# Optimization experiments

Hardware: AMD Instinct MI355X
Metric: run time of the kernel (lower is better)

## Reference

```python
import jax, jax.numpy as jnp
import numpy as np

B, S, D, H = 4, 8192, 256, 8

def setup_inputs() -> dict:
    key = jax.random.key(0)
    ks = jax.random.split(key, 6)
    return {
        "q": jax.random.normal(ks[0], (B, S, D), dtype=jnp.float32),
        "k": jax.random.normal(ks[1], (B, S, D), dtype=jnp.float32),
        "v": jax.random.normal(ks[2], (B, S, D), dtype=jnp.float32),
        "q_weights": jax.random.normal(ks[3], (H, D, D), dtype=jnp.float32),
        "k_weights": jax.random.normal(ks[4], (H, D, D), dtype=jnp.float32),
        "v_weights": jax.random.normal(ks[5], (H, D, D), dtype=jnp.float32),
    }

def reference(q, k, v, q_weights, k_weights, v_weights):
    # Faithful to the original: einsum 'bsd,hio->bhsd' shares no index between
    # the activation and the weight, so it is q[b,s,d] * sum_{i,o} W[h,i,o].
    qs = jax.nn.softmax(jnp.einsum('bsd,hio->bhsd', q, q_weights), axis=-2)  # softmax over s
    ks = jax.nn.softmax(jnp.einsum('bsd,hio->bhsd', k, k_weights), axis=-2)
    vs = jnp.einsum('bsd,hio->bhsd', v, v_weights)
    # 'bhnk,bhmv->bhkv': n and m are independently summed (outer product of seq-sums)
    global_contexts = jnp.einsum('bhnk,bhmv->bhkv', ks, vs)  # [b,h,d,d]
    # 'bhkv,bhsq->bhsv': k and q independently summed
    out = jnp.einsum('bhkv,bhsq->bhsv', global_contexts, qs)  # [b,h,s,d]
    # AdaptiveMaxPool2d((D,1)) on layout 'b s d h': identity over d (d==D), max over heads
    out = jnp.max(out, axis=1)  # [b,s,d]
    return out
```

## Files before the change

kernel.cpp:

```cpp
#include <hip/hip_runtime.h>

#define B 4
#define S 8192
#define D 256
#define H 8
#define NT 128
#define LOG2E 1.4426950408889634f
#define E2(x) __builtin_amdgcn_exp2f(x)

#define WS_WQ    0
#define WS_WV    8
#define WS_QMAX  16
#define WS_QMIN  (WS_QMAX + B*D)
#define WS_CV    (WS_QMIN + B*D)
#define WS_ZACC  (WS_CV + B*D)
#define WS_WP    (WS_ZACC + B*H*D)
#define WS_P1    (WS_WP + 1024)
#define WS_P2    (WS_P1 + B*NT*D)
#define WS_P3    (WS_P2 + B*NT*D)

__global__ __launch_bounds__(256) void kA(const float* __restrict__ q,
                                          const float* __restrict__ v,
                                          const float* __restrict__ qw,
                                          const float* __restrict__ vw,
                                          float* __restrict__ ws) {
    const int blk = blockIdx.x;
    const int t = threadIdx.x, w = t >> 6, lane = t & 63;

    if (blk >= B * NT) {
        const int i = blk - B * NT;
        const float4* src = (const float4*)(((i >> 7) ? vw : qw)
                              + (size_t)((i >> 4) & 7) * D * D) + (i & 15) * 1024;
        float sm = 0.f;
        #pragma unroll
        for (int j = 0; j < 4; ++j) {
            float4 a4 = src[j * 256 + t];
            sm += (a4.x + a4.y) + (a4.z + a4.w);
        }
        #pragma unroll
        for (int off = 32; off; off >>= 1) sm += __shfl_down(sm, off, 64);
        if (lane == 0) ws[WS_WP + i * 4 + w] = sm;
        return;
    }

    const int b = blk >> 7, tl = blk & (NT - 1);
    const int g = lane >> 4, cl = lane & 15;
    const int cblk = w * 16 + cl;
    const float4* qbase = (const float4*)(q + ((size_t)b * S + tl * 64) * D);
    const float4* vbase = (const float4*)(v + ((size_t)b * S + tl * 64) * D);
    float4 qmx = make_float4(-3.4e38f, -3.4e38f, -3.4e38f, -3.4e38f);
    float4 qmn = make_float4(3.4e38f, 3.4e38f, 3.4e38f, 3.4e38f);
    float4 vs = make_float4(0.f, 0.f, 0.f, 0.f);
    #pragma unroll 4
    for (int i = 0; i < 16; ++i) {
        const int row = i * 4 + g;
        float4 a4 = qbase[row * 64 + cblk];
        qmx.x = fmaxf(qmx.x, a4.x); qmx.y = fmaxf(qmx.y, a4.y);
        qmx.z = fmaxf(qmx.z, a4.z); qmx.w = fmaxf(qmx.w, a4.w);
        qmn.x = fminf(qmn.x, a4.x); qmn.y = fminf(qmn.y, a4.y);
        qmn.z = fminf(qmn.z, a4.z); qmn.w = fminf(qmn.w, a4.w);
        float4 b4 = vbase[row * 64 + cblk];
        vs.x += b4.x; vs.y += b4.y; vs.z += b4.z; vs.w += b4.w;
    }
    #pragma unroll
    for (int off = 16; off <= 32; off <<= 1) {
        qmx.x = fmaxf(qmx.x, __shfl_xor(qmx.x, off, 64));
        qmx.y = fmaxf(qmx.y, __shfl_xor(qmx.y, off, 64));
        qmx.z = fmaxf(qmx.z, __shfl_xor(qmx.z, off, 64));
        qmx.w = fmaxf(qmx.w, __shfl_xor(qmx.w, off, 64));
        qmn.x = fminf(qmn.x, __shfl_xor(qmn.x, off, 64));
        qmn.y = fminf(qmn.y, __shfl_xor(qmn.y, off, 64));
        qmn.z = fminf(qmn.z, __shfl_xor(qmn.z, off, 64));
        qmn.w = fminf(qmn.w, __shfl_xor(qmn.w, off, 64));
        vs.x += __shfl_xor(vs.x, off, 64);
        vs.y += __shfl_xor(vs.y, off, 64);
        vs.z += __shfl_xor(vs.z, off, 64);
        vs.w += __shfl_xor(vs.w, off, 64);
    }
    if (g == 0) {
        size_t pi = (size_t)(b * NT + tl) * D + cblk * 4;
        *(float4*)&ws[WS_P1 + pi] = qmx;
        *(float4*)&ws[WS_P2 + pi] = qmn;
        *(float4*)&ws[WS_P3 + pi] = vs;
    }
}

__global__ __launch_bounds__(256) void kB(float* __restrict__ ws) {
    const int blk = blockIdx.x, t = threadIdx.x;
    if (blk < 32) {
        const int bb = blk >> 3, oct = blk & 7;
        const int dl = t >> 3, sub = t & 7;
        const int d = oct * 32 + dl;
        float mx = -3.4e38f, mn = 3.4e38f, sm = 0.f;
        #pragma unroll 4
        for (int i = 0; i < 16; ++i) {
            size_t idx = (size_t)(bb * NT + sub * 16 + i) * D + d;
            mx = fmaxf(mx, ws[WS_P1 + idx]);
            mn = fminf(mn, ws[WS_P2 + idx]);
            sm += ws[WS_P3 + idx];
        }
        #pragma unroll
        for (int off = 1; off < 8; off <<= 1) {
            mx = fmaxf(mx, __shfl_xor(mx, off, 64));
            mn = fminf(mn, __shfl_xor(mn, off, 64));
            sm += __shfl_xor(sm, off, 64);
        }
        if (sub == 0) {
            ws[WS_QMAX + bb * D + d] = mx;
            ws[WS_QMIN + bb * D + d] = mn;
            ws[WS_CV + bb * D + d] = sm * (float)D;
        }
    } else if (blk == 32) {
        const int o = t >> 4, j = t & 15;
        float s = 0.f;
        #pragma unroll
        for (int ww = 0; ww < 4; ++ww) s += ws[WS_WP + (o * 16 + j) * 4 + ww];
        #pragma unroll
        for (int off = 1; off < 16; off <<= 1) s += __shfl_xor(s, off, 16);
        if (j == 0) ws[(o >= 8) ? (WS_WV + o - 8) : (WS_WQ + o)] = s;
    } else {
        #pragma unroll
        for (int e = 0; e < 8; ++e)
            *(float4*)&ws[WS_ZACC + e * 1024 + t * 4] = make_float4(0.f, 0.f, 0.f, 0.f);
    }
}

__global__ __launch_bounds__(256) void kC(const float* __restrict__ q,
                                          float* __restrict__ ws) {
    const int blk = blockIdx.x;
    const int b = blk >> 7, c = blk & 127;
    const int d = threadIdx.x;
    const float qmx = ws[WS_QMAX + b * D + d];
    const float qmn = ws[WS_QMIN + b * D + d];
    float a[H], cc[H], z[H];
    #pragma unroll
    for (int h = 0; h < H; ++h) {
        float wq_ = ws[WS_WQ + h];
        float M = (wq_ >= 0.f) ? wq_ * qmx : wq_ * qmn;
        a[h] = wq_ * LOG2E;
        cc[h] = -M * LOG2E;
        z[h] = 0.f;
    }
    const float* qp = q + ((size_t)b * S + c * 64) * D + d;
    #pragma unroll 4
    for (int r = 0; r < 64; ++r) {
        float qv = qp[(size_t)r * D];
        #pragma unroll
        for (int h = 0; h < H; ++h) z[h] += E2(fmaf(qv, a[h], cc[h]));
    }
    #pragma unroll
    for (int h = 0; h < H; ++h)
        atomicAdd(&ws[WS_ZACC + (size_t)(b * H + h) * D + d], z[h]);
}

__global__ __launch_bounds__(256, 8) void kE(const float* __restrict__ q,
                                             const float* __restrict__ ws,
                                             float* __restrict__ out) {
    __shared__ float kcs[H * D];
    __shared__ float wvs[8];

    const int blk = blockIdx.x;
    const int b = blk >> 9, tl = blk & 511;
    const int t = threadIdx.x, w = t >> 6, lane = t & 63;
    const int r = t >> 4, slice = t & 15;

    const float4* qp = (const float4*)(q + ((size_t)b * S + tl * 16 + r) * D
                                       + slice * 16);
    const float4 q0 = qp[0], q1 = qp[1], q2 = qp[2], q3 = qp[3];

    const int dst = ((t >> 2) & 3) * 64 + (t >> 4) * 4 + (t & 3);
    const float qmx = ws[WS_QMAX + b * D + t];
    const float qmn = ws[WS_QMIN + b * D + t];
    float a[H];
    #pragma unroll
    for (int h = 0; h < H; ++h) {
        const float wq_ = ws[WS_WQ + h];
        const float M = (wq_ >= 0.f) ? wq_ * qmx : wq_ * qmn;
        kcs[h * 256 + dst] = -M * LOG2E
            - __builtin_amdgcn_logf(ws[WS_ZACC + (size_t)(b * H + h) * D + t]);
        a[h] = wq_ * LOG2E;
    }
    if (t < 8) wvs[t] = ws[WS_WV + t];
    const float4 cv4 = *(const float4*)&ws[WS_CV + b * D + lane * 4];
    __syncthreads();

    float p[H];
    #pragma unroll
    for (int h = 0; h < H; ++h) p[h] = 0.f;

    const float4* kc4 = (const float4*)kcs;
    #pragma unroll
    for (int j = 0; j < 4; ++j) {
        const float4 qv = (j == 0) ? q0 : (j == 1) ? q1 : (j == 2) ? q2 : q3;
        #pragma unroll
        for (int h = 0; h < H; ++h) {
            const float4 k = kc4[h * 64 + j * 16 + slice];
            p[h] += (E2(fmaf(qv.x, a[h], k.x)) + E2(fmaf(qv.y, a[h], k.y)))
                  + (E2(fmaf(qv.z, a[h], k.z)) + E2(fmaf(qv.w, a[h], k.w)));
        }
    }
    #pragma unroll
    for (int st = 1; st < 16; st <<= 1) {
        #pragma unroll
        for (int h = 0; h < H; ++h) p[h] += __shfl_xor(p[h], st, 16);
    }
    float amax = -3.4e38f, amin = 3.4e38f;
    #pragma unroll
    for (int h = 0; h < H; ++h) {
        const float A = wvs[h] * p[h];
        amax = fmaxf(amax, A);
        amin = fminf(amin, A);
    }

    float* og = out + ((size_t)b * S + tl * 16 + w * 4) * D;
    #pragma unroll
    for (int rr = 0; rr < 4; ++rr) {
        const float am = __shfl(amax, rr * 16, 64);
        const float an = __shfl(amin, rr * 16, 64);
        float4 o;
        o.x = (cv4.x >= 0.f) ? cv4.x * am : cv4.x * an;
        o.y = (cv4.y >= 0.f) ? cv4.y * am : cv4.y * an;
        o.z = (cv4.z >= 0.f) ? cv4.z * am : cv4.z * an;
        o.w = (cv4.w >= 0.f) ? cv4.w * am : cv4.w * an;
        *(float4*)&og[(size_t)rr * D + lane * 4] = o;
    }
}

extern "C" void kernel_launch(void* const* d_in, const int* in_sizes, int n_in,
                              void* d_out, int out_size, void* d_ws, size_t ws_size,
                              hipStream_t stream) {
    const float* q  = (const float*)d_in[0];
    const float* v  = (const float*)d_in[2];
    const float* qw = (const float*)d_in[3];
    const float* vw = (const float*)d_in[5];
    float* out = (float*)d_out;
    float* ws  = (float*)d_ws;

    kA<<<B * NT + 256, 256, 0, stream>>>(q, v, qw, vw, ws);
    kB<<<34, 256, 0, stream>>>(ws);
    kC<<<512, 256, 0, stream>>>(q, ws);
    kE<<<B * 512, 256, 0, stream>>>(q, ws, out);
}
```

Before: 51.69 us.

## Replace reduction kernel with order-preserving atomics and double rows per block in kE

Drops the separate reduction kernel kB: kA now folds per-tile q max/min into global results with atomicMax on an order-preserving unsigned encoding of floats, and folds v sums and weight sums with atomicAdd. A memset zeroes the accumulators first. kE now handles 32 rows per block in two groups, reusing the per-block shared setup (log of the normalizers) across twice as many rows. The trade is atomic contention on a small set of addresses and more work per block in kE, with fewer blocks in flight.

```diff
diff --git a/kernel.cpp b/kernel.cpp
--- a/kernel.cpp
+++ b/kernel.cpp
@@ -4,20 +4,24 @@
 #define S 8192
 #define D 256
 #define H 8
-#define NT 128
 #define LOG2E 1.4426950408889634f
 #define E2(x) __builtin_amdgcn_exp2f(x)
 
 #define WS_WQ    0
 #define WS_WV    8
-#define WS_QMAX  16
-#define WS_QMIN  (WS_QMAX + B*D)
-#define WS_CV    (WS_QMIN + B*D)
+#define WS_QMAXE 16
+#define WS_QMINE (WS_QMAXE + B*D)
+#define WS_CV    (WS_QMINE + B*D)
 #define WS_ZACC  (WS_CV + B*D)
-#define WS_WP    (WS_ZACC + B*H*D)
-#define WS_P1    (WS_WP + 1024)
-#define WS_P2    (WS_P1 + B*NT*D)
-#define WS_P3    (WS_P2 + B*NT*D)
+#define WS_END   (WS_ZACC + B*H*D)
+
+__device__ __forceinline__ unsigned enc(float x) {
+    unsigned u = __float_as_uint(x);
+    return (u >> 31) ? ~u : (u | 0x80000000u);
+}
+__device__ __forceinline__ float dec(unsigned e) {
+    return (e >> 31) ? __uint_as_float(e & 0x7FFFFFFFu) : __uint_as_float(~e);
+}
 
 __global__ __launch_bounds__(256) void kA(const float* __restrict__ q,
                                           const float* __restrict__ v,
@@ -27,10 +31,11 @@
     const int blk = blockIdx.x;
     const int t = threadIdx.x, w = t >> 6, lane = t & 63;
 
-    if (blk >= B * NT) {
-        const int i = blk - B * NT;
+    if (blk >= 512) {
+        const int i = blk - 512;
+        const int h = (i >> 4) & 7;
         const float4* src = (const float4*)(((i >> 7) ? vw : qw)
-                              + (size_t)((i >> 4) & 7) * D * D) + (i & 15) * 1024;
+                              + (size_t)h * D * D) + (i & 15) * 1024;
         float sm = 0.f;
         #pragma unroll
         for (int j = 0; j < 4; ++j) {
@@ -39,11 +44,16 @@
         }
         #pragma unroll
         for (int off = 32; off; off >>= 1) sm += __shfl_down(sm, off, 64);
-        if (lane == 0) ws[WS_WP + i * 4 + w] = sm;
+        __shared__ float red[4];
+        if (lane == 0) red[w] = sm;
+        __syncthreads();
+        if (t == 0)
+            atomicAdd(&ws[((i >> 7) ? WS_WV : WS_WQ) + h],
+                      (red[0] + red[1]) + (red[2] + red[3]));
         return;
     }
 
-    const int b = blk >> 7, tl = blk & (NT - 1);
+    const int b = blk >> 7, tl = blk & 127;
     const int g = lane >> 4, cl = lane & 15;
     const int cblk = w * 16 + cl;
     const float4* qbase = (const float4*)(q + ((size_t)b * S + tl * 64) * D);
@@ -78,50 +88,17 @@
         vs.w += __shfl_xor(vs.w, off, 64);
     }
     if (g == 0) {
-        size_t pi = (size_t)(b * NT + tl) * D + cblk * 4;
-        *(float4*)&ws[WS_P1 + pi] = qmx;
-        *(float4*)&ws[WS_P2 + pi] = qmn;
-        *(float4*)&ws[WS_P3 + pi] = vs;
-    }
-}
-
-__global__ __launch_bounds__(256) void kB(float* __restrict__ ws) {
-    const int blk = blockIdx.x, t = threadIdx.x;
-    if (blk < 32) {
-        const int bb = blk >> 3, oct = blk & 7;
-        const int dl = t >> 3, sub = t & 7;
-        const int d = oct * 32 + dl;
-        float mx = -3.4e38f, mn = 3.4e38f, sm = 0.f;
-        #pragma unroll 4
-        for (int i = 0; i < 16; ++i) {
-            size_t idx = (size_t)(bb * NT + sub * 16 + i) * D + d;
-            mx = fmaxf(mx, ws[WS_P1 + idx]);
-            mn = fminf(mn, ws[WS_P2 + idx]);
-            sm += ws[WS_P3 + idx];
-        }
-        #pragma unroll
-        for (int off = 1; off < 8; off <<= 1) {
-            mx = fmaxf(mx, __shfl_xor(mx, off, 64));
-            mn = fminf(mn, __shfl_xor(mn, off, 64));
-            sm += __shfl_xor(sm, off, 64);
-        }
-        if (sub == 0) {
-            ws[WS_QMAX + bb * D + d] = mx;
-            ws[WS_QMIN + bb * D + d] = mn;
-            ws[WS_CV + bb * D + d] = sm * (float)D;
-        }
-    } else if (blk == 32) {
-        const int o = t >> 4, j = t & 15;
-        float s = 0.f;
-        #pragma unroll
-        for (int ww = 0; ww < 4; ++ww) s += ws[WS_WP + (o * 16 + j) * 4 + ww];
-        #pragma unroll
-        for (int off = 1; off < 16; off <<= 1) s += __shfl_xor(s, off, 16);
-        if (j == 0) ws[(o >= 8) ? (WS_WV + o - 8) : (WS_WQ + o)] = s;
-    } else {
-        #pragma unroll
-        for (int e = 0; e < 8; ++e)
-            *(float4*)&ws[WS_ZACC + e * 1024 + t * 4] = make_float4(0.f, 0.f, 0.f, 0.f);
+        const int d0 = b * D + cblk * 4;
+        unsigned* qme = (unsigned*)&ws[WS_QMAXE + d0];
+        unsigned* qne = (unsigned*)&ws[WS_QMINE + d0];
+        atomicMax(&qme[0], enc(qmx.x)); atomicMax(&qme[1], enc(qmx.y));
+        atomicMax(&qme[2], enc(qmx.z)); atomicMax(&qme[3], enc(qmx.w));
+        atomicMax(&qne[0], enc(-qmn.x)); atomicMax(&qne[1], enc(-qmn.y));
+        atomicMax(&qne[2], enc(-qmn.z)); atomicMax(&qne[3], enc(-qmn.w));
+        atomicAdd(&ws[WS_CV + d0 + 0], vs.x);
+        atomicAdd(&ws[WS_CV + d0 + 1], vs.y);
+        atomicAdd(&ws[WS_CV + d0 + 2], vs.z);
+        atomicAdd(&ws[WS_CV + d0 + 3], vs.w);
     }
 }
 
@@ -130,8 +107,8 @@
     const int blk = blockIdx.x;
     const int b = blk >> 7, c = blk & 127;
     const int d = threadIdx.x;
-    const float qmx = ws[WS_QMAX + b * D + d];
-    const float qmn = ws[WS_QMIN + b * D + d];
+    const float qmx = dec(((const unsigned*)&ws[WS_QMAXE])[b * D + d]);
+    const float qmn = -dec(((const unsigned*)&ws[WS_QMINE])[b * D + d]);
     float a[H], cc[H], z[H];
     #pragma unroll
     for (int h = 0; h < H; ++h) {
@@ -160,17 +137,17 @@
     __shared__ float wvs[8];
 
     const int blk = blockIdx.x;
-    const int b = blk >> 9, tl = blk & 511;
+    const int b = blk >> 8, tl = blk & 255;
     const int t = threadIdx.x, w = t >> 6, lane = t & 63;
     const int r = t >> 4, slice = t & 15;
 
-    const float4* qp = (const float4*)(q + ((size_t)b * S + tl * 16 + r) * D
-                                       + slice * 16);
-    const float4 q0 = qp[0], q1 = qp[1], q2 = qp[2], q3 = qp[3];
+    const float* qbase = q + ((size_t)b * S + tl * 32 + r) * D + slice * 16;
+    const float4* qp1 = (const float4*)qbase;
+    const float4 q0 = qp1[0], q1 = qp1[1], q2 = qp1[2], q3 = qp1[3];
 
     const int dst = ((t >> 2) & 3) * 64 + (t >> 4) * 4 + (t & 3);
-    const float qmx = ws[WS_QMAX + b * D + t];
-    const float qmn = ws[WS_QMIN + b * D + t];
+    const float qmx = dec(((const unsigned*)&ws[WS_QMAXE])[b * D + t]);
+    const float qmn = -dec(((const unsigned*)&ws[WS_QMINE])[b * D + t]);
     float a[H];
     #pragma unroll
     for (int h = 0; h < H; ++h) {
@@ -180,49 +157,58 @@
             - __builtin_amdgcn_logf(ws[WS_ZACC + (size_t)(b * H + h) * D + t]);
         a[h] = wq_ * LOG2E;
     }
-    if (t < 8) wvs[t] = ws[WS_WV + t];
+    if (t < 8) wvs[t] = ws[WS_WV + t] * (float)D;
     const float4 cv4 = *(const float4*)&ws[WS_CV + b * D + lane * 4];
     __syncthreads();
 
-    float p[H];
-    #pragma unroll
-    for (int h = 0; h < H; ++h) p[h] = 0.f;
-
     const float4* kc4 = (const float4*)kcs;
-    #pragma unroll
-    for (int j = 0; j < 4; ++j) {
-        const float4 qv = (j == 0) ? q0 : (j == 1) ? q1 : (j == 2) ? q2 : q3;
+    float* og = out + ((size_t)b * S + tl * 32 + w * 4) * D;
+
+    #pragma unroll
+    for (int grp = 0; grp < 2; ++grp) {
+        float4 g0, g1, g2, g3;
+        if (grp == 0) { g0 = q0; g1 = q1; g2 = q2; g3 = q3; }
+        else {
+            const float4* qp2 = (const float4*)(qbase + 16 * D);
+            g0 = qp2[0]; g1 = qp2[1]; g2 = qp2[2]; g3 = qp2[3];
+        }
+        float p[H];
+        #pragma unroll
+        for (int h = 0; h < H; ++h) p[h] = 0.f;
+        #pragma unroll
+        for (int j = 0; j < 4; ++j) {
+            const float4 qv = (j == 0) ? g0 : (j == 1) ? g1 : (j == 2) ? g2 : g3;
+            #pragma unroll
+            for (int h = 0; h < H; ++h) {
+                const float4 k = kc4[h * 64 + j * 16 + slice];
+                p[h] += (E2(fmaf(qv.x, a[h], k.x)) + E2(fmaf(qv.y, a[h], k.y)))
+                      + (E2(fmaf(qv.z, a[h], k.z)) + E2(fmaf(qv.w, a[h], k.w)));
+            }
+        }
+        #pragma unroll
+        for (int st = 1; st < 16; st <<= 1) {
+            #pragma unroll
+            for (int h = 0; h < H; ++h) p[h] += __shfl_xor(p[h], st, 16);
+        }
+        float amax = -3.4e38f, amin = 3.4e38f;
         #pragma unroll
         for (int h = 0; h < H; ++h) {
-            const float4 k = kc4[h * 64 + j * 16 + slice];
-            p[h] += (E2(fmaf(qv.x, a[h], k.x)) + E2(fmaf(qv.y, a[h], k.y)))
-                  + (E2(fmaf(qv.z, a[h], k.z)) + E2(fmaf(qv.w, a[h], k.w)));
-        }
-    }
-    #pragma unroll
-    for (int st = 1; st < 16; st <<= 1) {
-        #pragma unroll
-        for (int h = 0; h < H; ++h) p[h] += __shfl_xor(p[h], st, 16);
-    }
-    float amax = -3.4e38f, amin = 3.4e38f;
-    #pragma unroll
-    for (int h = 0; h < H; ++h) {
-        const float A = wvs[h] * p[h];
-        amax = fmaxf(amax, A);
-        amin = fminf(amin, A);
-    }
-
-    float* og = out + ((size_t)b * S + tl * 16 + w * 4) * D;
-    #pragma unroll
-    for (int rr = 0; rr < 4; ++rr) {
-        const float am = __shfl(amax, rr * 16, 64);
-        const float an = __shfl(amin, rr * 16, 64);
-        float4 o;
-        o.x = (cv4.x >= 0.f) ? cv4.x * am : cv4.x * an;
-        o.y = (cv4.y >= 0.f) ? cv4.y * am : cv4.y * an;
-        o.z = (cv4.z >= 0.f) ? cv4.z * am : cv4.z * an;
-        o.w = (cv4.w >= 0.f) ? cv4.w * am : cv4.w * an;
-        *(float4*)&og[(size_t)rr * D + lane * 4] = o;
+            const float A = wvs[h] * p[h];
+            amax = fmaxf(amax, A);
+            amin = fminf(amin, A);
+        }
+        float* ogr = og + (size_t)grp * 16 * D;
+        #pragma unroll
+        for (int rr = 0; rr < 4; ++rr) {
+            const float am = __shfl(amax, rr * 16, 64);
+            const float an = __shfl(amin, rr * 16, 64);
+            float4 o;
+            o.x = (cv4.x >= 0.f) ? cv4.x * am : cv4.x * an;
+            o.y = (cv4.y >= 0.f) ? cv4.y * am : cv4.y * an;
+            o.z = (cv4.z >= 0.f) ? cv4.z * am : cv4.z * an;
+            o.w = (cv4.w >= 0.f) ? cv4.w * am : cv4.w * an;
+            *(float4*)&ogr[(size_t)rr * D + lane * 4] = o;
+        }
     }
 }
 
@@ -236,8 +222,8 @@
     float* out = (float*)d_out;
     float* ws  = (float*)d_ws;
 
-    kA<<<B * NT + 256, 256, 0, stream>>>(q, v, qw, vw, ws);
-    kB<<<34, 256, 0, stream>>>(ws);
+    hipMemsetAsync(ws, 0, WS_END * sizeof(float), stream);
+    kA<<<768, 256, 0, stream>>>(q, v, qw, vw, ws);
     kC<<<512, 256, 0, stream>>>(q, ws);
-    kE<<<B * 512, 256, 0, stream>>>(q, ws, out);
-}
+    kE<<<B * 256, 256, 0, stream>>>(q, ws, out);
+}
```

Measured after the change: 188.4 us. +264.4%, slower.
